# Kernel optimization log

Hardware: AMD Instinct MI355X
Metric: run time of the kernel (lower is better)

## Reference

```python
import jax, jax.numpy as jnp
import numpy as np

B, S, D = 4, 2048, 1024
NEG_BIG = -1.0e9


def setup_inputs() -> dict:
    key = jax.random.key(0)
    ks = jax.random.split(key, 9)
    scale = 1.0 / np.sqrt(D)
    inp = {
        "v": jax.random.normal(ks[0], (B, S, D), dtype=jnp.float32),
        "k": jax.random.normal(ks[1], (B, S, D), dtype=jnp.float32),
        "q": jax.random.normal(ks[2], (B, S, D), dtype=jnp.float32),
        # causal mask: 1 where attention is disallowed (j > i), broadcast over batch
        "mask": jnp.triu(jnp.ones((1, S, S), dtype=jnp.float32), k=1),
        "Wq": jax.random.normal(ks[3], (D, D), dtype=jnp.float32) * scale,
        "bq": jnp.zeros((D,), dtype=jnp.float32),
        "Wk": jax.random.normal(ks[4], (D, D), dtype=jnp.float32) * scale,
        "bk": jnp.zeros((D,), dtype=jnp.float32),
        "Wv": jax.random.normal(ks[5], (D, D), dtype=jnp.float32) * scale,
        "bv": jnp.zeros((D,), dtype=jnp.float32),
    }
    return inp


def reference(v, k, q, mask, Wq, bq, Wk, bk, Wv, bv):
    # Dense projections (Keras Dense: x @ W + b)
    qp = q @ Wq + bq  # [B, S, D]
    kp = k @ Wk + bk  # [B, S, D]
    vp = v @ Wv + bv  # [B, S, D]

    dk = jnp.asarray(D, dtype=qp.dtype)
    logits = jnp.einsum("bqd,bkd->bqk", qp, kp) / jnp.sqrt(dk)  # [B, S, S]
    logits = logits + mask * NEG_BIG
    attn = jax.nn.softmax(logits, axis=-1)  # [B, S, S]
    out = jnp.einsum("bqk,bkd->bqd", attn, vp)  # [B, S, D]
    return out, attn
```

## Files before the change

kernel.cpp:

```cpp
#include <hip/hip_runtime.h>
#include <hip/hip_bf16.h>
#include <cstdint>

#define BATCH 4
#define S_LEN 2048
#define D_DIM 1024

typedef __attribute__((ext_vector_type(4))) float f32x4_t;
typedef __attribute__((ext_vector_type(8))) __bf16 bf16x8_t;

__device__ __forceinline__ ushort f32_to_bf16(float f) {
    uint32_t u = __float_as_uint(f);
    uint32_t r = (u + 0x7FFFu + ((u >> 16) & 1u)) >> 16;
    return (ushort)r;
}

__global__ __launch_bounds__(256)
void cvt3_kernel(const float* __restrict__ a, const float* __restrict__ b,
                 const float* __restrict__ c, ushort* __restrict__ out, int n4) {
    int z = blockIdx.y;
    const float* src = (z == 0) ? a : ((z == 1) ? b : c);
    ushort* dst = out + (size_t)z * n4 * 4;
    int idx = blockIdx.x * blockDim.x + threadIdx.x;
    int stride = gridDim.x * blockDim.x;
    const float4* in4 = (const float4*)src;
    ushort4* out4 = (ushort4*)dst;
    for (int i = idx; i < n4; i += stride) {
        float4 v = in4[i];
        ushort4 o;
        o.x = f32_to_bf16(v.x);
        o.y = f32_to_bf16(v.y);
        o.z = f32_to_bf16(v.z);
        o.w = f32_to_bf16(v.w);
        out4[i] = o;
    }
}

__global__ __launch_bounds__(256)
void transpose_cvt_kernel(const float* __restrict__ in, ushort* __restrict__ out,
                          int rows, int cols) {
    __shared__ ushort tile[64][66];
    int r0 = blockIdx.y * 64, c0 = blockIdx.x * 64;
    int t = threadIdx.x;
    int cr = t & 63;
    int cc = t >> 6;
    #pragma unroll
    for (int i = 0; i < 16; ++i) {
        int r = cc * 16 + i;
        tile[r][cr] = f32_to_bf16(in[(size_t)(r0 + r) * cols + (c0 + cr)]);
    }
    __syncthreads();
    #pragma unroll
    for (int i = 0; i < 16; ++i) {
        int c = cc * 16 + i;
        out[(size_t)(c0 + c) * rows + (r0 + cr)] = tile[cr][c];
    }
}

__global__ __launch_bounds__(256)
void transpose_bf16_kernel(const ushort* __restrict__ in, ushort* __restrict__ out,
                           int rows, int cols, int lda, long strideA, long strideB) {
    __shared__ ushort tile[64][66];
    const ushort* src = in + (size_t)blockIdx.z * strideA;
    ushort* dst = out + (size_t)blockIdx.z * strideB;
    int r0 = blockIdx.y * 64, c0 = blockIdx.x * 64;
    int t = threadIdx.x;
    int cr = t & 63;
    int cc = t >> 6;
    #pragma unroll
    for (int i = 0; i < 16; ++i) {
        int r = cc * 16 + i;
        tile[r][cr] = src[(size_t)(r0 + r) * lda + (c0 + cr)];
    }
    __syncthreads();
    #pragma unroll
    for (int i = 0; i < 16; ++i) {
        int c = cc * 16 + i;
        dst[(size_t)(c0 + c) * rows + (r0 + cr)] = tile[cr][c];
    }
}

__global__ __launch_bounds__(256)
void bias_concat_kernel(const float* __restrict__ bq, const float* __restrict__ bk,
                        const float* __restrict__ bv, float* __restrict__ out) {
    int i = blockIdx.x * blockDim.x + threadIdx.x;
    if (i < D_DIM) out[i] = bq[i];
    else if (i < 2 * D_DIM) out[i] = bk[i - D_DIM];
    else if (i < 3 * D_DIM) out[i] = bv[i - 2 * D_DIM];
}

enum { MODE_PROJ = 0, MODE_LOGITS = 1, MODE_OUT = 2 };

#define PRE_BAR() do { __builtin_amdgcn_sched_barrier(0); __builtin_amdgcn_s_barrier(); \
    asm volatile("s_waitcnt lgkmcnt(0)" ::: "memory"); __builtin_amdgcn_sched_barrier(0); } while (0)
#define POST_BAR() do { __builtin_amdgcn_sched_barrier(0); __builtin_amdgcn_s_barrier(); } while (0)
#define GATE(N) do { asm volatile("s_waitcnt vmcnt(" #N ")" ::: "memory"); \
    __builtin_amdgcn_sched_barrier(0); } while (0)

__device__ __forceinline__ void xcd_swizzle(int& bc, int& br) {
    int gx = gridDim.x;
    int nwg = gx * gridDim.y;
    int orig = blockIdx.y * gx + blockIdx.x;
    int xcd = orig & 7, idx = orig >> 3;
    int q8 = nwg >> 3, r8 = nwg & 7;
    int wgid = (xcd < r8 ? xcd * (q8 + 1) : r8 * (q8 + 1) + (xcd - r8) * q8) + idx;
    bc = wgid % gx;
    br = wgid / gx;
}

__global__ __launch_bounds__(512, 2)
void gemm_proj_kernel(const ushort* __restrict__ A, const ushort* __restrict__ Bt,
                      const float* __restrict__ bias, ushort* __restrict__ Cout,
                      int K, int lda, int ldb, int ldc, long strideA) {
    __shared__ ushort As[2][256 * 64];
    __shared__ ushort Bs[2][256 * 64];
    int bc, br;
    xcd_swizzle(bc, br);
    const ushort* Ab = A + (size_t)(bc >> 2) * strideA;
    const ushort* Bb = Bt;
    int brow = br * 256, bcol = bc * 256;
    int t = threadIdx.x, lane = t & 63, wid = t >> 6;
    int wr = wid >> 2, wc = wid & 3;
    int nkt = K / 64, niter = nkt >> 1;

    auto stageA = [&](int tk, int half) {
        ushort* dst = &As[tk & 1][0];
        #pragma unroll
        for (int j = 0; j < 2; ++j) {
            int o = half * 16384 + (j * 512 + t) * 16;
            int row = o >> 7;
            int col = (o & 127) ^ ((row & 7) << 4);
            const ushort* src = Ab + (size_t)(brow + row) * lda + tk * 64 + (col >> 1);
            __builtin_amdgcn_global_load_lds(
                (const __attribute__((address_space(1))) uint32_t*)src,
                (__attribute__((address_space(3))) uint32_t*)(dst + (o >> 1)), 16, 0, 0);
        }
    };
    auto stageB = [&](int tk, int half) {
        ushort* dst = &Bs[tk & 1][0];
        #pragma unroll
        for (int j = 0; j < 2; ++j) {
            int o = half * 16384 + (j * 512 + t) * 16;
            int row = o >> 7;
            int col = (o & 127) ^ ((row & 7) << 4);
            const ushort* src = Bb + (size_t)(bcol + row) * ldb + tk * 64 + (col >> 1);
            __builtin_amdgcn_global_load_lds(
                (const __attribute__((address_space(1))) uint32_t*)src,
                (__attribute__((address_space(3))) uint32_t*)(dst + (o >> 1)), 16, 0, 0);
        }
    };

    f32x4_t acc[8][4];
    #pragma unroll
    for (int m = 0; m < 8; ++m)
        #pragma unroll
        for (int n = 0; n < 4; ++n)
            acc[m][n] = (f32x4_t){0.f, 0.f, 0.f, 0.f};

    bf16x8_t afl[4][2], afh[4][2], bfr[4][2];

    auto readAhalf = [&](int tk, int mh, bf16x8_t (&dst)[4][2]) {
        const char* base = (const char*)&As[tk & 1][0];
        #pragma unroll
        for (int m = 0; m < 4; ++m) {
            int ra = wr * 128 + mh * 64 + m * 16 + (lane & 15);
            int sw = (ra & 7) << 4;
            #pragma unroll
            for (int ks = 0; ks < 2; ++ks) {
                int cb = ks * 64 + ((lane >> 4) * 16);
                dst[m][ks] = *(const bf16x8_t*)(base + ra * 128 + (cb ^ sw));
            }
        }
    };
    auto readB = [&](int tk) {
        const char* base = (const char*)&Bs[tk & 1][0];
        #pragma unroll
        for (int n = 0; n < 4; ++n) {
            int rb = wc * 64 + n * 16 + (lane & 15);
            int sw = (rb & 7) << 4;
            #pragma unroll
            for (int ks = 0; ks < 2; ++ks) {
                int cb = ks * 64 + ((lane >> 4) * 16);
                bfr[n][ks] = *(const bf16x8_t*)(base + rb * 128 + (cb ^ sw));
            }
        }
    };

#define QUAD66(AF, MH, NH)                                                          \
    do { __builtin_amdgcn_s_setprio(1);                                             \
        _Pragma("unroll") for (int m = 0; m < 4; ++m)                               \
        _Pragma("unroll") for (int n = 0; n < 2; ++n)                               \
        _Pragma("unroll") for (int ks = 0; ks < 2; ++ks)                            \
            acc[(MH) * 4 + m][(NH) * 2 + n] = __builtin_amdgcn_mfma_f32_16x16x32_bf16( \
                AF[m][ks], bfr[(NH) * 2 + n][ks], acc[(MH) * 4 + m][(NH) * 2 + n], 0, 0, 0); \
        __builtin_amdgcn_s_setprio(0); } while (0)

    stageA(0, 0); stageA(0, 1); stageB(0, 0); stageB(0, 1);
    stageA(1, 0); stageA(1, 1);
    GATE(4);
    __builtin_amdgcn_s_barrier();

    for (int i = 0; i < niter; ++i) {
        int t2 = 2 * i, u = 2 * i + 1;
        bool smid = (t2 + 2 < nkt);
        readAhalf(t2, 0, afl); readB(t2);
        stageB(u, 0);
        PRE_BAR(); QUAD66(afl, 0, 0); POST_BAR();
        readAhalf(t2, 1, afh);
        stageB(u, 1);
        PRE_BAR(); QUAD66(afl, 0, 1); POST_BAR();
        if (smid) stageA(t2 + 2, 0);
        PRE_BAR(); QUAD66(afh, 1, 0); POST_BAR();
        if (smid) stageA(t2 + 2, 1);
        PRE_BAR(); QUAD66(afh, 1, 1);
        if (smid) { GATE(4); } else { GATE(0); }
        POST_BAR();
        readAhalf(u, 0, afl); readB(u);
        if (smid) stageB(t2 + 2, 0);
        PRE_BAR(); QUAD66(afl, 0, 0); POST_BAR();
        readAhalf(u, 1, afh);
        if (smid) stageB(t2 + 2, 1);
        PRE_BAR(); QUAD66(afl, 0, 1); POST_BAR();
        if (smid) stageA(u + 2, 0);
        PRE_BAR(); QUAD66(afh, 1, 0); POST_BAR();
        if (smid) stageA(u + 2, 1);
        PRE_BAR(); QUAD66(afh, 1, 1);
        if (smid) { GATE(4); } else { GATE(0); }
        POST_BAR();
    }
#undef QUAD66

    int crow0 = brow + wr * 128 + ((lane >> 4) * 4);
    int ccol0 = bcol + wc * 64 + (lane & 15);
    #pragma unroll
    for (int mf = 0; mf < 8; ++mf) {
        #pragma unroll
        for (int nf = 0; nf < 4; ++nf) {
            int col = ccol0 + nf * 16;
            float bv = bias[col];
            #pragma unroll
            for (int j = 0; j < 4; ++j) {
                int rowg = crow0 + mf * 16 + j;
                Cout[(size_t)rowg * ldc + col] = f32_to_bf16(acc[mf][nf][j] + bv);
            }
        }
    }
}

template<int MODE>
__global__ __launch_bounds__(512, 2)
void gemm_128_kernel(const ushort* __restrict__ A, const ushort* __restrict__ Bt,
                     float* __restrict__ Cout,
                     int K, int lda, int ldb, int ldc,
                     long strideA, long strideB, long strideC, float scale) {
    __shared__ ushort As[2][256 * 64];
    __shared__ ushort Bs[2][128 * 64];
    int bc, br;
    xcd_swizzle(bc, br);
    int bz = blockIdx.z;
    if (MODE == MODE_LOGITS && bc > 2 * br + 1) return;
    const ushort* Ab = A + (size_t)bz * strideA;
    const ushort* Bb = Bt + (size_t)bz * strideB;
    int brow = br * 256, bcol = bc * 128;
    int t = threadIdx.x, lane = t & 63, wid = t >> 6;
    int wr = wid >> 1, wc = wid & 1;
    int nkt = K / 64;
    if (MODE == MODE_OUT) nkt = min(nkt, (brow + 256) / 64);
    int niter = nkt >> 1;

    auto stageA = [&](int tk, int half) {
        ushort* dst = &As[tk & 1][0];
        #pragma unroll
        for (int j = 0; j < 2; ++j) {
            int o = half * 16384 + (j * 512 + t) * 16;
            int row = o >> 7;
            int col = (o & 127) ^ ((row & 7) << 4);
            const ushort* src = Ab + (size_t)(brow + row) * lda + tk * 64 + (col >> 1);
            __builtin_amdgcn_global_load_lds(
                (const __attribute__((address_space(1))) uint32_t*)src,
                (__attribute__((address_space(3))) uint32_t*)(dst + (o >> 1)), 16, 0, 0);
        }
    };
    auto stageB = [&](int tk) {
        ushort* dst = &Bs[tk & 1][0];
        #pragma unroll
        for (int j = 0; j < 2; ++j) {
            int o = (j * 512 + t) * 16;
            int row = o >> 7;
            int col = (o & 127) ^ ((row & 7) << 4);
            const ushort* src = Bb + (size_t)(bcol + row) * ldb + tk * 64 + (col >> 1);
            __builtin_amdgcn_global_load_lds(
                (const __attribute__((address_space(1))) uint32_t*)src,
                (__attribute__((address_space(3))) uint32_t*)(dst + (o >> 1)), 16, 0, 0);
        }
    };

    f32x4_t acc[4][4];
    #pragma unroll
    for (int m = 0; m < 4; ++m)
        #pragma unroll
        for (int n = 0; n < 4; ++n)
            acc[m][n] = (f32x4_t){0.f, 0.f, 0.f, 0.f};

    bf16x8_t af[4][2], bfr[4][2];

    auto readAll = [&](int tk) {
        const char* baseA = (const char*)&As[tk & 1][0];
        #pragma unroll
        for (int m = 0; m < 4; ++m) {
            int ra = wr * 64 + m * 16 + (lane & 15);
            int sw = (ra & 7) << 4;
            #pragma unroll
            for (int ks = 0; ks < 2; ++ks) {
                int cb = ks * 64 + ((lane >> 4) * 16);
                af[m][ks] = *(const bf16x8_t*)(baseA + ra * 128 + (cb ^ sw));
            }
        }
        const char* baseB = (const char*)&Bs[tk & 1][0];
        #pragma unroll
        for (int n = 0; n < 4; ++n) {
            int rb = wc * 64 + n * 16 + (lane & 15);
            int sw = (rb & 7) << 4;
            #pragma unroll
            for (int ks = 0; ks < 2; ++ks) {
                int cb = ks * 64 + ((lane >> 4) * 16);
                bfr[n][ks] = *(const bf16x8_t*)(baseB + rb * 128 + (cb ^ sw));
            }
        }
    };

#define QUAD28(MH, NH)                                                              \
    do { __builtin_amdgcn_s_setprio(1);                                             \
        _Pragma("unroll") for (int m = 0; m < 2; ++m)                               \
        _Pragma("unroll") for (int n = 0; n < 2; ++n)                               \
        _Pragma("unroll") for (int ks = 0; ks < 2; ++ks)                            \
            acc[(MH) * 2 + m][(NH) * 2 + n] = __builtin_amdgcn_mfma_f32_16x16x32_bf16( \
                af[(MH) * 2 + m][ks], bfr[(NH) * 2 + n][ks], acc[(MH) * 2 + m][(NH) * 2 + n], 0, 0, 0); \
        __builtin_amdgcn_s_setprio(0); } while (0)

    stageA(0, 0); stageA(0, 1); stageB(0);
    stageA(1, 0); stageA(1, 1); stageB(1);
    GATE(6);
    __builtin_amdgcn_s_barrier();

    for (int i = 0; i < niter; ++i) {
        int t2 = 2 * i, u = 2 * i + 1;
        bool smid = (t2 + 2 < nkt);
        readAll(t2);
        PRE_BAR(); QUAD28(0, 0); POST_BAR();
        PRE_BAR(); QUAD28(0, 1); POST_BAR();
        if (smid) stageA(t2 + 2, 0);
        PRE_BAR(); QUAD28(1, 0); POST_BAR();
        if (smid) stageA(t2 + 2, 1);
        PRE_BAR(); QUAD28(1, 1);
        if (smid) { GATE(4); } else { GATE(0); }
        POST_BAR();
        readAll(u);
        if (smid) stageB(t2 + 2);
        PRE_BAR(); QUAD28(0, 0); POST_BAR();
        if (smid) stageA(u + 2, 0);
        PRE_BAR(); QUAD28(0, 1); POST_BAR();
        if (smid) stageA(u + 2, 1);
        PRE_BAR(); QUAD28(1, 0); POST_BAR();
        if (smid) stageB(u + 2);
        PRE_BAR(); QUAD28(1, 1);
        if (smid) { GATE(6); } else { GATE(0); }
        POST_BAR();
    }
#undef QUAD28

    float* C = Cout + (size_t)bz * strideC;
    int crow0 = brow + wr * 64 + ((lane >> 4) * 4);
    int ccol0 = bcol + wc * 64 + (lane & 15);
    #pragma unroll
    for (int mf = 0; mf < 4; ++mf)
        #pragma unroll
        for (int nf = 0; nf < 4; ++nf) {
            int col = ccol0 + nf * 16;
            #pragma unroll
            for (int j = 0; j < 4; ++j) {
                int rowg = crow0 + mf * 16 + j;
                C[(size_t)rowg * ldc + col] = acc[mf][nf][j] * scale;
            }
        }
}

__global__ __launch_bounds__(256)
void softmax_causal_kernel(float* __restrict__ attn, ushort* __restrict__ attn_bf) {
    int rowid = blockIdx.x;
    int i = rowid & (S_LEN - 1);
    float* lrow = attn + (size_t)rowid * S_LEN;
    ushort* brw = attn_bf + (size_t)rowid * S_LEN;
    int t = threadIdx.x;
    int nvalid = i + 1;

    float vals[8];
    float lmax = -1e30f;
    #pragma unroll
    for (int it = 0; it < 8; ++it) {
        int j = it * 256 + t;
        float v = (j < nvalid) ? lrow[j] : -1e30f;
        vals[it] = v;
        lmax = fmaxf(lmax, v);
    }
    #pragma unroll
    for (int off = 32; off > 0; off >>= 1)
        lmax = fmaxf(lmax, __shfl_xor(lmax, off));

    __shared__ float redm[4];
    __shared__ float reds[4];
    int wave = t >> 6, lane = t & 63;
    if (lane == 0) redm[wave] = lmax;
    __syncthreads();
    float m = fmaxf(fmaxf(redm[0], redm[1]), fmaxf(redm[2], redm[3]));

    float lsum = 0.f;
    #pragma unroll
    for (int it = 0; it < 8; ++it) {
        int j = it * 256 + t;
        float e = (j < nvalid) ? __expf(vals[it] - m) : 0.f;
        vals[it] = e;
        lsum += e;
    }
    #pragma unroll
    for (int off = 32; off > 0; off >>= 1)
        lsum += __shfl_xor(lsum, off);
    if (lane == 0) reds[wave] = lsum;
    __syncthreads();
    float denom = reds[0] + reds[1] + reds[2] + reds[3];
    float inv = 1.f / denom;

    #pragma unroll
    for (int it = 0; it < 8; ++it) {
        int j = it * 256 + t;
        float p = vals[it] * inv;
        lrow[j] = p;
        brw[j] = f32_to_bf16(p);
    }
}

extern "C" void kernel_launch(void* const* d_in, const int* in_sizes, int n_in,
                              void* d_out, int out_size, void* d_ws, size_t ws_size,
                              hipStream_t stream) {
    const float* v  = (const float*)d_in[0];
    const float* k  = (const float*)d_in[1];
    const float* q  = (const float*)d_in[2];
    const float* Wq = (const float*)d_in[4];
    const float* bq = (const float*)d_in[5];
    const float* Wk = (const float*)d_in[6];
    const float* bk = (const float*)d_in[7];
    const float* Wv = (const float*)d_in[8];
    const float* bv = (const float*)d_in[9];

    float* out  = (float*)d_out;
    float* attn = (float*)d_out + (size_t)BATCH * S_LEN * D_DIM;

    char* ws = (char*)d_ws;
    const size_t NTOK = (size_t)BATCH * S_LEN;
    const size_t XSZ  = NTOK * D_DIM * sizeof(ushort);
    ushort* xqkv  = (ushort*)(ws);
    ushort* qkvp  = (ushort*)(ws + 3 * XSZ);
    ushort* WT    = (ushort*)(ws + 6 * XSZ);
    float*  bias3 = (float*)(ws + 6 * XSZ + 3 * (size_t)D_DIM * D_DIM * sizeof(ushort));
    ushort* vpT     = (ushort*)(ws);
    ushort* attn_bf = (ushort*)(ws + XSZ);

    const int n4 = (int)(NTOK * D_DIM / 4);
    cvt3_kernel<<<dim3(1024, 3), dim3(256), 0, stream>>>(q, k, v, xqkv, n4);

    transpose_cvt_kernel<<<dim3(16, 16), dim3(256), 0, stream>>>(Wq, WT, D_DIM, D_DIM);
    transpose_cvt_kernel<<<dim3(16, 16), dim3(256), 0, stream>>>(Wk, WT + (size_t)D_DIM * D_DIM, D_DIM, D_DIM);
    transpose_cvt_kernel<<<dim3(16, 16), dim3(256), 0, stream>>>(Wv, WT + 2 * (size_t)D_DIM * D_DIM, D_DIM, D_DIM);
    bias_concat_kernel<<<dim3(12), dim3(256), 0, stream>>>(bq, bk, bv, bias3);

    gemm_proj_kernel<<<dim3(12, 32, 1), dim3(512), 0, stream>>>(
        xqkv, WT, bias3, qkvp, D_DIM, D_DIM, D_DIM, 3 * D_DIM, (long)NTOK * D_DIM);

    transpose_bf16_kernel<<<dim3(D_DIM / 64, S_LEN / 64, BATCH), dim3(256), 0, stream>>>(
        qkvp + 2 * D_DIM, vpT, S_LEN, D_DIM, 3 * D_DIM,
        (long)S_LEN * 3 * D_DIM, (long)D_DIM * S_LEN);

    gemm_128_kernel<MODE_LOGITS><<<dim3(16, 8, BATCH), dim3(512), 0, stream>>>(
        qkvp, qkvp + D_DIM, attn, D_DIM, 3 * D_DIM, 3 * D_DIM, S_LEN,
        (long)S_LEN * 3 * D_DIM, (long)S_LEN * 3 * D_DIM, (long)S_LEN * S_LEN, 0.03125f);

    softmax_causal_kernel<<<dim3((int)NTOK), dim3(256), 0, stream>>>(attn, attn_bf);

    gemm_128_kernel<MODE_OUT><<<dim3(8, 8, BATCH), dim3(512), 0, stream>>>(
        attn_bf, vpT, out, S_LEN, S_LEN, S_LEN, D_DIM,
        (long)S_LEN * S_LEN, (long)D_DIM * S_LEN, (long)S_LEN * D_DIM, 1.f);
}
```

Baseline: 242.6 us.

## Restructure GEMM main loops with split A-fragment reads and whole-tile staging

Both GEMM kernels now issue global-to-LDS staging for a whole A or B tile at once, at different points in the MFMA quad schedule, and move the vmcnt gate to before the last quad instead of inside it. The projection kernel drops its double A-fragment registers (afl/afh) and rereads A halves just in time, which lowers register pressure. The logits/out kernel splits A reads into halves in the same way. The XCD swizzle is simplified by dropping the remainder handling, which is only correct when the workgroup count is a multiple of 8. The change trades register savings against more exposed LDS read latency and a different load-overlap pattern.

```diff
diff --git a/kernel.cpp b/kernel.cpp
--- a/kernel.cpp
+++ b/kernel.cpp
@@ -91,19 +91,23 @@
 
 enum { MODE_PROJ = 0, MODE_LOGITS = 1, MODE_OUT = 2 };
 
-#define PRE_BAR() do { __builtin_amdgcn_sched_barrier(0); __builtin_amdgcn_s_barrier(); \
-    asm volatile("s_waitcnt lgkmcnt(0)" ::: "memory"); __builtin_amdgcn_sched_barrier(0); } while (0)
-#define POST_BAR() do { __builtin_amdgcn_sched_barrier(0); __builtin_amdgcn_s_barrier(); } while (0)
-#define GATE(N) do { asm volatile("s_waitcnt vmcnt(" #N ")" ::: "memory"); \
+#define PRE_BAR() do { __builtin_amdgcn_s_barrier(); \
+    asm volatile("s_waitcnt lgkmcnt(0)" ::: "memory"); \
     __builtin_amdgcn_sched_barrier(0); } while (0)
+#define POST_BAR() do { __builtin_amdgcn_sched_barrier(0); \
+    __builtin_amdgcn_s_barrier(); } while (0)
+#define GATE(N) asm volatile("s_waitcnt vmcnt(" #N ")" ::: "memory")
+
+#define GLOAD(dst, src) __builtin_amdgcn_global_load_lds( \
+    (const __attribute__((address_space(1))) uint32_t*)(src), \
+    (__attribute__((address_space(3))) uint32_t*)(dst), 16, 0, 0)
 
 __device__ __forceinline__ void xcd_swizzle(int& bc, int& br) {
     int gx = gridDim.x;
     int nwg = gx * gridDim.y;
     int orig = blockIdx.y * gx + blockIdx.x;
     int xcd = orig & 7, idx = orig >> 3;
-    int q8 = nwg >> 3, r8 = nwg & 7;
-    int wgid = (xcd < r8 ? xcd * (q8 + 1) : r8 * (q8 + 1) + (xcd - r8) * q8) + idx;
+    int wgid = xcd * (nwg >> 3) + idx;
     bc = wgid % gx;
     br = wgid / gx;
 }
@@ -123,30 +127,24 @@
     int wr = wid >> 2, wc = wid & 3;
     int nkt = K / 64, niter = nkt >> 1;
 
-    auto stageA = [&](int tk, int half) {
+    auto stageA = [&](int tk) {
         ushort* dst = &As[tk & 1][0];
         #pragma unroll
-        for (int j = 0; j < 2; ++j) {
-            int o = half * 16384 + (j * 512 + t) * 16;
+        for (int j = 0; j < 4; ++j) {
+            int o = (j * 512 + t) * 16;
             int row = o >> 7;
             int col = (o & 127) ^ ((row & 7) << 4);
-            const ushort* src = Ab + (size_t)(brow + row) * lda + tk * 64 + (col >> 1);
-            __builtin_amdgcn_global_load_lds(
-                (const __attribute__((address_space(1))) uint32_t*)src,
-                (__attribute__((address_space(3))) uint32_t*)(dst + (o >> 1)), 16, 0, 0);
-        }
-    };
-    auto stageB = [&](int tk, int half) {
+            GLOAD(dst + (o >> 1), Ab + (size_t)(brow + row) * lda + tk * 64 + (col >> 1));
+        }
+    };
+    auto stageB = [&](int tk) {
         ushort* dst = &Bs[tk & 1][0];
         #pragma unroll
-        for (int j = 0; j < 2; ++j) {
-            int o = half * 16384 + (j * 512 + t) * 16;
+        for (int j = 0; j < 4; ++j) {
+            int o = (j * 512 + t) * 16;
             int row = o >> 7;
             int col = (o & 127) ^ ((row & 7) << 4);
-            const ushort* src = Bb + (size_t)(bcol + row) * ldb + tk * 64 + (col >> 1);
-            __builtin_amdgcn_global_load_lds(
-                (const __attribute__((address_space(1))) uint32_t*)src,
-                (__attribute__((address_space(3))) uint32_t*)(dst + (o >> 1)), 16, 0, 0);
+            GLOAD(dst + (o >> 1), Bb + (size_t)(bcol + row) * ldb + tk * 64 + (col >> 1));
         }
     };
 
@@ -157,9 +155,9 @@
         for (int n = 0; n < 4; ++n)
             acc[m][n] = (f32x4_t){0.f, 0.f, 0.f, 0.f};
 
-    bf16x8_t afl[4][2], afh[4][2], bfr[4][2];
-
-    auto readAhalf = [&](int tk, int mh, bf16x8_t (&dst)[4][2]) {
+    bf16x8_t af[4][2], bfr[4][2];
+
+    auto readA = [&](int tk, int mh) {
         const char* base = (const char*)&As[tk & 1][0];
         #pragma unroll
         for (int m = 0; m < 4; ++m) {
@@ -168,7 +166,7 @@
             #pragma unroll
             for (int ks = 0; ks < 2; ++ks) {
                 int cb = ks * 64 + ((lane >> 4) * 16);
-                dst[m][ks] = *(const bf16x8_t*)(base + ra * 128 + (cb ^ sw));
+                af[m][ks] = *(const bf16x8_t*)(base + ra * 128 + (cb ^ sw));
             }
         }
     };
@@ -186,49 +184,42 @@
         }
     };
 
-#define QUAD66(AF, MH, NH)                                                          \
+#define PQUAD(MH, NH)                                                               \
     do { __builtin_amdgcn_s_setprio(1);                                             \
         _Pragma("unroll") for (int m = 0; m < 4; ++m)                               \
         _Pragma("unroll") for (int n = 0; n < 2; ++n)                               \
         _Pragma("unroll") for (int ks = 0; ks < 2; ++ks)                            \
             acc[(MH) * 4 + m][(NH) * 2 + n] = __builtin_amdgcn_mfma_f32_16x16x32_bf16( \
-                AF[m][ks], bfr[(NH) * 2 + n][ks], acc[(MH) * 4 + m][(NH) * 2 + n], 0, 0, 0); \
+                af[m][ks], bfr[(NH) * 2 + n][ks], acc[(MH) * 4 + m][(NH) * 2 + n], 0, 0, 0); \
         __builtin_amdgcn_s_setprio(0); } while (0)
 
-    stageA(0, 0); stageA(0, 1); stageB(0, 0); stageB(0, 1);
-    stageA(1, 0); stageA(1, 1);
-    GATE(4);
+    stageB(0); stageA(0); stageB(1); stageA(1);
+    GATE(8);
     __builtin_amdgcn_s_barrier();
 
     for (int i = 0; i < niter; ++i) {
         int t2 = 2 * i, u = 2 * i + 1;
         bool smid = (t2 + 2 < nkt);
-        readAhalf(t2, 0, afl); readB(t2);
-        stageB(u, 0);
-        PRE_BAR(); QUAD66(afl, 0, 0); POST_BAR();
-        readAhalf(t2, 1, afh);
-        stageB(u, 1);
-        PRE_BAR(); QUAD66(afl, 0, 1); POST_BAR();
-        if (smid) stageA(t2 + 2, 0);
-        PRE_BAR(); QUAD66(afh, 1, 0); POST_BAR();
-        if (smid) stageA(t2 + 2, 1);
-        PRE_BAR(); QUAD66(afh, 1, 1);
-        if (smid) { GATE(4); } else { GATE(0); }
-        POST_BAR();
-        readAhalf(u, 0, afl); readB(u);
-        if (smid) stageB(t2 + 2, 0);
-        PRE_BAR(); QUAD66(afl, 0, 0); POST_BAR();
-        readAhalf(u, 1, afh);
-        if (smid) stageB(t2 + 2, 1);
-        PRE_BAR(); QUAD66(afl, 0, 1); POST_BAR();
-        if (smid) stageA(u + 2, 0);
-        PRE_BAR(); QUAD66(afh, 1, 0); POST_BAR();
-        if (smid) stageA(u + 2, 1);
-        PRE_BAR(); QUAD66(afh, 1, 1);
-        if (smid) { GATE(4); } else { GATE(0); }
-        POST_BAR();
-    }
-#undef QUAD66
+        readA(t2, 0); readB(t2);
+        PRE_BAR(); PQUAD(0, 0); POST_BAR();
+        if (smid) stageB(t2 + 2);
+        PRE_BAR(); PQUAD(0, 1); POST_BAR();
+        readA(t2, 1);
+        PRE_BAR(); PQUAD(1, 0); POST_BAR();
+        if (smid) stageA(t2 + 2);
+        if (smid) { GATE(8); } else { GATE(0); }
+        PRE_BAR(); PQUAD(1, 1); POST_BAR();
+        readA(u, 0); readB(u);
+        PRE_BAR(); PQUAD(0, 0); POST_BAR();
+        if (smid) stageB(u + 2);
+        PRE_BAR(); PQUAD(0, 1); POST_BAR();
+        readA(u, 1);
+        PRE_BAR(); PQUAD(1, 0); POST_BAR();
+        if (smid) stageA(u + 2);
+        if (smid) { GATE(8); } else { GATE(0); }
+        PRE_BAR(); PQUAD(1, 1); POST_BAR();
+    }
+#undef PQUAD
 
     int crow0 = brow + wr * 128 + ((lane >> 4) * 4);
     int ccol0 = bcol + wc * 64 + (lane & 15);
@@ -268,17 +259,14 @@
     if (MODE == MODE_OUT) nkt = min(nkt, (brow + 256) / 64);
     int niter = nkt >> 1;
 
-    auto stageA = [&](int tk, int half) {
+    auto stageA = [&](int tk) {
         ushort* dst = &As[tk & 1][0];
         #pragma unroll
-        for (int j = 0; j < 2; ++j) {
-            int o = half * 16384 + (j * 512 + t) * 16;
+        for (int j = 0; j < 4; ++j) {
+            int o = (j * 512 + t) * 16;
             int row = o >> 7;
             int col = (o & 127) ^ ((row & 7) << 4);
-            const ushort* src = Ab + (size_t)(brow + row) * lda + tk * 64 + (col >> 1);
-            __builtin_amdgcn_global_load_lds(
-                (const __attribute__((address_space(1))) uint32_t*)src,
-                (__attribute__((address_space(3))) uint32_t*)(dst + (o >> 1)), 16, 0, 0);
+            GLOAD(dst + (o >> 1), Ab + (size_t)(brow + row) * lda + tk * 64 + (col >> 1));
         }
     };
     auto stageB = [&](int tk) {
@@ -288,10 +276,7 @@
             int o = (j * 512 + t) * 16;
             int row = o >> 7;
             int col = (o & 127) ^ ((row & 7) << 4);
-            const ushort* src = Bb + (size_t)(bcol + row) * ldb + tk * 64 + (col >> 1);
-            __builtin_amdgcn_global_load_lds(
-                (const __attribute__((address_space(1))) uint32_t*)src,
-                (__attribute__((address_space(3))) uint32_t*)(dst + (o >> 1)), 16, 0, 0);
+            GLOAD(dst + (o >> 1), Bb + (size_t)(bcol + row) * ldb + tk * 64 + (col >> 1));
         }
     };
 
@@ -302,21 +287,23 @@
         for (int n = 0; n < 4; ++n)
             acc[m][n] = (f32x4_t){0.f, 0.f, 0.f, 0.f};
 
-    bf16x8_t af[4][2], bfr[4][2];
-
-    auto readAll = [&](int tk) {
-        const char* baseA = (const char*)&As[tk & 1][0];
-        #pragma unroll
-        for (int m = 0; m < 4; ++m) {
-            int ra = wr * 64 + m * 16 + (lane & 15);
+    bf16x8_t af[2][2], bfr[4][2];
+
+    auto readA = [&](int tk, int mh) {
+        const char* base = (const char*)&As[tk & 1][0];
+        #pragma unroll
+        for (int m = 0; m < 2; ++m) {
+            int ra = wr * 64 + mh * 32 + m * 16 + (lane & 15);
             int sw = (ra & 7) << 4;
             #pragma unroll
             for (int ks = 0; ks < 2; ++ks) {
                 int cb = ks * 64 + ((lane >> 4) * 16);
-                af[m][ks] = *(const bf16x8_t*)(baseA + ra * 128 + (cb ^ sw));
-            }
-        }
-        const char* baseB = (const char*)&Bs[tk & 1][0];
+                af[m][ks] = *(const bf16x8_t*)(base + ra * 128 + (cb ^ sw));
+            }
+        }
+    };
+    auto readB = [&](int tk) {
+        const char* base = (const char*)&Bs[tk & 1][0];
         #pragma unroll
         for (int n = 0; n < 4; ++n) {
             int rb = wc * 64 + n * 16 + (lane & 15);
@@ -324,50 +311,47 @@
             #pragma unroll
             for (int ks = 0; ks < 2; ++ks) {
                 int cb = ks * 64 + ((lane >> 4) * 16);
-                bfr[n][ks] = *(const bf16x8_t*)(baseB + rb * 128 + (cb ^ sw));
-            }
-        }
-    };
-
-#define QUAD28(MH, NH)                                                              \
+                bfr[n][ks] = *(const bf16x8_t*)(base + rb * 128 + (cb ^ sw));
+            }
+        }
+    };
+
+#define PQUAD(MH, NH)                                                               \
     do { __builtin_amdgcn_s_setprio(1);                                             \
         _Pragma("unroll") for (int m = 0; m < 2; ++m)                               \
         _Pragma("unroll") for (int n = 0; n < 2; ++n)                               \
         _Pragma("unroll") for (int ks = 0; ks < 2; ++ks)                            \
             acc[(MH) * 2 + m][(NH) * 2 + n] = __builtin_amdgcn_mfma_f32_16x16x32_bf16( \
-                af[(MH) * 2 + m][ks], bfr[(NH) * 2 + n][ks], acc[(MH) * 2 + m][(NH) * 2 + n], 0, 0, 0); \
+                af[m][ks], bfr[(NH) * 2 + n][ks], acc[(MH) * 2 + m][(NH) * 2 + n], 0, 0, 0); \
         __builtin_amdgcn_s_setprio(0); } while (0)
 
-    stageA(0, 0); stageA(0, 1); stageB(0);
-    stageA(1, 0); stageA(1, 1); stageB(1);
+    stageB(0); stageA(0); stageB(1); stageA(1);
     GATE(6);
     __builtin_amdgcn_s_barrier();
 
     for (int i = 0; i < niter; ++i) {
         int t2 = 2 * i, u = 2 * i + 1;
         bool smid = (t2 + 2 < nkt);
-        readAll(t2);
-        PRE_BAR(); QUAD28(0, 0); POST_BAR();
-        PRE_BAR(); QUAD28(0, 1); POST_BAR();
-        if (smid) stageA(t2 + 2, 0);
-        PRE_BAR(); QUAD28(1, 0); POST_BAR();
-        if (smid) stageA(t2 + 2, 1);
-        PRE_BAR(); QUAD28(1, 1);
-        if (smid) { GATE(4); } else { GATE(0); }
-        POST_BAR();
-        readAll(u);
+        readA(t2, 0); readB(t2);
+        PRE_BAR(); PQUAD(0, 0); POST_BAR();
         if (smid) stageB(t2 + 2);
-        PRE_BAR(); QUAD28(0, 0); POST_BAR();
-        if (smid) stageA(u + 2, 0);
-        PRE_BAR(); QUAD28(0, 1); POST_BAR();
-        if (smid) stageA(u + 2, 1);
-        PRE_BAR(); QUAD28(1, 0); POST_BAR();
+        PRE_BAR(); PQUAD(0, 1); POST_BAR();
+        readA(t2, 1);
+        PRE_BAR(); PQUAD(1, 0); POST_BAR();
+        if (smid) stageA(t2 + 2);
+        if (smid) { GATE(6); } else { GATE(0); }
+        PRE_BAR(); PQUAD(1, 1); POST_BAR();
+        readA(u, 0); readB(u);
+        PRE_BAR(); PQUAD(0, 0); POST_BAR();
         if (smid) stageB(u + 2);
-        PRE_BAR(); QUAD28(1, 1);
+        PRE_BAR(); PQUAD(0, 1); POST_BAR();
+        readA(u, 1);
+        PRE_BAR(); PQUAD(1, 0); POST_BAR();
+        if (smid) stageA(u + 2);
         if (smid) { GATE(6); } else { GATE(0); }
-        POST_BAR();
-    }
-#undef QUAD28
+        PRE_BAR(); PQUAD(1, 1); POST_BAR();
+    }
+#undef PQUAD
 
     float* C = Cout + (size_t)bz * strideC;
     int crow0 = brow + wr * 64 + ((lane >> 4) * 4);
```

New measurement: 226.7 us. -6.5%, faster.
